# Optimization experiments

Measured on AMD Instinct MI355X. Metric: run time of the kernel, lower is better.

## Reference

```python
import jax, jax.numpy as jnp
import numpy as np

K = 3  # kernel_size

def setup_inputs() -> dict:
    key = jax.random.key(0)
    k1, k2, k3 = jax.random.split(key, 3)
    B, C, H, W = 8, 64, 128, 128
    x = jax.random.normal(k1, (B, C, H, W), dtype=jnp.float32)
    # 1x1 conv weight (out_channels*K*K, in_channels) and bias
    W_gen = jax.random.normal(k2, (C * K * K, C), dtype=jnp.float32) / np.float32(np.sqrt(C))
    b_gen = jax.random.normal(k3, (C * K * K,), dtype=jnp.float32) * 0.01
    return {"x": x, "W_gen": W_gen, "b_gen": b_gen}

def reference(x, W_gen, b_gen):
    B, C, H, W = x.shape  # out_channels == in_channels (required by the view)
    # filter_gen: 1x1 conv + ReLU -> (B, C*K*K, H, W)
    f = jax.nn.relu(jnp.einsum('bchw,oc->bohw', x, W_gen) + b_gen[None, :, None, None])
    filters = f.reshape(B, C, K * K, H, W)
    # F.unfold with padding=(K-1)//2, stride 1: gather KxK patches per pixel.
    pad = (K - 1) // 2
    xp = jnp.pad(x, ((0, 0), (0, 0), (pad, pad), (pad, pad)))
    # kernel-position index runs row-major (i*K + j), matching unfold layout
    patches = jnp.stack([xp[:, :, i:i + H, j:j + W]
                         for i in range(K) for j in range(K)], axis=2)  # (B,C,K*K,H,W)
    out = (filters * patches).sum(axis=2)  # (B,C,H,W)
    return out
```

## Files before the change

kernel.cpp:

```cpp
#include <hip/hip_runtime.h>
#include <hip/hip_bf16.h>

#define CC 64
#define HH 128
#define WW 128
#define OO 576
#define HW (HH * WW)

typedef __attribute__((ext_vector_type(8))) short short8;
typedef __attribute__((ext_vector_type(4))) short short4v;
typedef __attribute__((ext_vector_type(4))) float floatx4;

__device__ __forceinline__ unsigned short f2bf(float f) {
    unsigned u = __float_as_uint(f);
    u = (u + 0x7FFFu + ((u >> 16) & 1u)) >> 16;
    return (unsigned short)u;
}

__device__ __forceinline__ float bf2f(short s) {
    return __uint_as_float(((unsigned)(unsigned short)s) << 16);
}

__device__ __forceinline__ short8 pack8(floatx4 a, floatx4 b) {
    __hip_bfloat162 p0 = __float22bfloat162_rn(make_float2(a[0], a[1]));
    __hip_bfloat162 p1 = __float22bfloat162_rn(make_float2(a[2], a[3]));
    __hip_bfloat162 p2 = __float22bfloat162_rn(make_float2(b[0], b[1]));
    __hip_bfloat162 p3 = __float22bfloat162_rn(make_float2(b[2], b[3]));
    unsigned u0, u1, u2, u3;
    __builtin_memcpy(&u0, &p0, 4); __builtin_memcpy(&u1, &p1, 4);
    __builtin_memcpy(&u2, &p2, 4); __builtin_memcpy(&u3, &p3, 4);
    short8 v;
    v[0] = (short)(u0 & 0xffffu); v[1] = (short)(u0 >> 16);
    v[2] = (short)(u1 & 0xffffu); v[3] = (short)(u1 >> 16);
    v[4] = (short)(u2 & 0xffffu); v[5] = (short)(u2 >> 16);
    v[6] = (short)(u3 & 0xffffu); v[7] = (short)(u3 >> 16);
    return v;
}

__global__ void ACDA_wconv_kernel(const float* __restrict__ Wg,
                                  const float* __restrict__ bg,
                                  unsigned short* __restrict__ Wb,
                                  float* __restrict__ Bp) {
    int i = blockIdx.x * 256 + threadIdx.x;
    if (i < OO * CC) {
        int o2  = i >> 6;
        int col = i & 63;
        int kk  = o2 >> 6;
        int c   = o2 & 63;
        Wb[i] = f2bf(Wg[(c * 9 + kk) * CC + col]);
    }
    if (i < OO) Bp[i] = bg[(i & 63) * 9 + (i >> 6)];
}

__global__ __launch_bounds__(512, 4) void ACDA_main_kernel(
    const float* __restrict__ x, const unsigned short* __restrict__ Wb,
    const float* __restrict__ Bp, float* __restrict__ out)
{
    __shared__ short S[4][66][72];

    const int tid  = threadIdx.x;
    const int lane = tid & 63;
    const int g    = tid >> 6;
    const int hw   = g & 1;
    const int cg   = g >> 1;
    const int quad = lane >> 4;
    const int l16  = lane & 15;
    const int c0   = cg * 16;

    const int bid = blockIdx.x;
    const int wk  = (bid & 7) * 128 + (bid >> 3);
    const int seg = wk & 1;
    const int hp  = (wk >> 1) & 63;
    const int b   = wk >> 7;
    const int w0  = seg << 6;
    const int h0  = hp << 1;

    const float* xb = x + (size_t)b * CC * HW;

#pragma unroll
    for (int r = 0; r < 4; ++r) {
        const int hh = h0 + r - 1;
        const bool oob = (hh < 0) || (hh > 127);
        const int hc = hh < 0 ? 0 : (hh > 127 ? 127 : hh);
        const float* src = xb + hc * WW + w0 + lane;
        const int c = g * 8;
        short8 v8 = short8{0, 0, 0, 0, 0, 0, 0, 0};
        if (!oob) {
            floatx4 va, vb;
            va[0] = src[(c + 0) * HW]; va[1] = src[(c + 1) * HW];
            va[2] = src[(c + 2) * HW]; va[3] = src[(c + 3) * HW];
            vb[0] = src[(c + 4) * HW]; vb[1] = src[(c + 5) * HW];
            vb[2] = src[(c + 6) * HW]; vb[3] = src[(c + 7) * HW];
            v8 = pack8(va, vb);
        }
        *(short8*)&S[r][lane + 1][c] = v8;
    }
    {
        const int r4   = tid >> 7;
        const int idx  = tid & 127;
        const int c    = idx >> 1;
        const int side = idx & 1;
        const int hh = h0 + r4 - 1;
        const bool oob = (hh < 0) || (hh > 127);
        const int hc = hh < 0 ? 0 : (hh > 127 ? 127 : hh);
        const int col = side ? (w0 + 64) : (w0 - 1);
        unsigned short v = 0;
        if (!oob && col >= 0 && col < WW)
            v = f2bf(xb[c * HW + hc * WW + col]);
        S[r4][side ? 65 : 0][c] = (short)v;
    }
    __syncthreads();

    short8 bfrag[4][2];
#pragma unroll
    for (int nt = 0; nt < 4; ++nt)
#pragma unroll
        for (int ks = 0; ks < 2; ++ks) {
            bfrag[nt][ks] = *(const short8*)&S[hw + 1][nt * 16 + l16 + 1][ks * 32 + quad * 8];
            asm volatile("" : "+v"(bfrag[nt][ks]));
        }

    floatx4 acc[4];
#pragma unroll
    for (int nt = 0; nt < 4; ++nt) acc[nt] = floatx4{0.f, 0.f, 0.f, 0.f};

#pragma unroll
    for (int t = 0; t < 9; ++t) {
        const int di = t / 3;
        const int dj = t - 3 * di;
        const unsigned short* wrow = Wb + (t * 64 + c0 + l16) * CC + quad * 8;
        short8 a0 = *(const short8*)(wrow);
        short8 a1 = *(const short8*)(wrow + 32);
        floatx4 bv = *(const floatx4*)(Bp + t * 64 + c0 + 4 * quad);
#pragma unroll
        for (int nt = 0; nt < 4; ++nt) {
            short4v ph = *(const short4v*)&S[hw + di][nt * 16 + l16 + dj][c0 + 4 * quad];
            floatx4 z = bv;
            z = __builtin_amdgcn_mfma_f32_16x16x32_bf16(a0, bfrag[nt][0], z, 0, 0, 0);
            z = __builtin_amdgcn_mfma_f32_16x16x32_bf16(a1, bfrag[nt][1], z, 0, 0, 0);
#pragma unroll
            for (int rg = 0; rg < 4; ++rg)
                acc[nt][rg] = fmaf(fmaxf(z[rg], 0.f), bf2f(ph[rg]), acc[nt][rg]);
        }
    }

    float* ob = out + (size_t)b * CC * HW + (h0 + hw) * WW + w0;
#pragma unroll
    for (int nt = 0; nt < 4; ++nt)
#pragma unroll
        for (int rg = 0; rg < 4; ++rg)
            ob[(c0 + 4 * quad + rg) * HW + nt * 16 + l16] = acc[nt][rg];
}

extern "C" void kernel_launch(void* const* d_in, const int* in_sizes, int n_in,
                              void* d_out, int out_size, void* d_ws, size_t ws_size,
                              hipStream_t stream) {
    const float* x  = (const float*)d_in[0];
    const float* Wg = (const float*)d_in[1];
    const float* bg = (const float*)d_in[2];
    float* out = (float*)d_out;
    unsigned short* Wb = (unsigned short*)d_ws;
    float* Bp = (float*)((char*)d_ws + OO * CC * 2);

    ACDA_wconv_kernel<<<dim3((OO * CC + 255) / 256), dim3(256), 0, stream>>>(Wg, bg, Wb, Bp);
    ACDA_main_kernel<<<dim3(8 * 64 * 2), dim3(512), 0, stream>>>(x, Wb, Bp, out);
}
```

Before: 108.2 us.

## Pre-transpose input to channels-last bf16 in a fused prep kernel

A preprocessing kernel now converts x from NCHW fp32 to NHWC bf16 in workspace, using a shared-memory transpose. The same launch also handles the weight and bias reordering. The main kernel then stages its halo tile with contiguous 16-byte loads instead of strided per-channel fp32 gathers and per-element halo loads. This costs an extra full read and write of x (in bf16) through global memory, which the main kernel's cheaper, more coalesced loads must outweigh.

```diff
diff --git a/kernel.cpp b/kernel.cpp
--- a/kernel.cpp
+++ b/kernel.cpp
@@ -10,6 +10,7 @@
 typedef __attribute__((ext_vector_type(8))) short short8;
 typedef __attribute__((ext_vector_type(4))) short short4v;
 typedef __attribute__((ext_vector_type(4))) float floatx4;
+typedef __attribute__((ext_vector_type(4))) unsigned int uint4v;
 
 __device__ __forceinline__ unsigned short f2bf(float f) {
     unsigned u = __float_as_uint(f);
@@ -21,39 +22,56 @@
     return __uint_as_float(((unsigned)(unsigned short)s) << 16);
 }
 
-__device__ __forceinline__ short8 pack8(floatx4 a, floatx4 b) {
-    __hip_bfloat162 p0 = __float22bfloat162_rn(make_float2(a[0], a[1]));
-    __hip_bfloat162 p1 = __float22bfloat162_rn(make_float2(a[2], a[3]));
-    __hip_bfloat162 p2 = __float22bfloat162_rn(make_float2(b[0], b[1]));
-    __hip_bfloat162 p3 = __float22bfloat162_rn(make_float2(b[2], b[3]));
-    unsigned u0, u1, u2, u3;
-    __builtin_memcpy(&u0, &p0, 4); __builtin_memcpy(&u1, &p1, 4);
-    __builtin_memcpy(&u2, &p2, 4); __builtin_memcpy(&u3, &p3, 4);
-    short8 v;
-    v[0] = (short)(u0 & 0xffffu); v[1] = (short)(u0 >> 16);
-    v[2] = (short)(u1 & 0xffffu); v[3] = (short)(u1 >> 16);
-    v[4] = (short)(u2 & 0xffffu); v[5] = (short)(u2 >> 16);
-    v[6] = (short)(u3 & 0xffffu); v[7] = (short)(u3 >> 16);
-    return v;
-}
+__global__ __launch_bounds__(256) void ACDA_pre_kernel(
+    const float* __restrict__ x, const float* __restrict__ Wg,
+    const float* __restrict__ bg, unsigned short* __restrict__ Wb,
+    float* __restrict__ Bp, unsigned short* __restrict__ xbf)
+{
+    const int bid = blockIdx.x, tid = threadIdx.x;
+    if (bid >= 1024) {
+        int i = (bid - 1024) * 256 + tid;
+        if (i < OO * CC) {
+            int o2  = i >> 6;
+            int col = i & 63;
+            int kk  = o2 >> 6;
+            int c   = o2 & 63;
+            Wb[i] = f2bf(Wg[(c * 9 + kk) * CC + col]);
+        }
+        if (i < OO) Bp[i] = bg[(i & 63) * 9 + (i >> 6)];
+        return;
+    }
+    const int b = bid >> 7, h = bid & 127;
+    __shared__ float T[64][132];
 
-__global__ void ACDA_wconv_kernel(const float* __restrict__ Wg,
-                                  const float* __restrict__ bg,
-                                  unsigned short* __restrict__ Wb,
-                                  float* __restrict__ Bp) {
-    int i = blockIdx.x * 256 + threadIdx.x;
-    if (i < OO * CC) {
-        int o2  = i >> 6;
-        int col = i & 63;
-        int kk  = o2 >> 6;
-        int c   = o2 & 63;
-        Wb[i] = f2bf(Wg[(c * 9 + kk) * CC + col]);
+    {
+        const int c = tid >> 2, q = tid & 3;
+        const float* sp = x + ((size_t)(b * CC + c) * HH + h) * WW + q * 32;
+#pragma unroll
+        for (int j = 0; j < 8; ++j)
+            *(floatx4*)&T[c][q * 32 + 4 * j] = *(const floatx4*)(sp + 4 * j);
     }
-    if (i < OO) Bp[i] = bg[(i & 63) * 9 + (i >> 6)];
+    __syncthreads();
+    {
+        const int w = tid >> 1, half = tid & 1;
+        unsigned u[16];
+#pragma unroll
+        for (int k = 0; k < 16; ++k) {
+            float f0 = T[half * 32 + 2 * k][w];
+            float f1 = T[half * 32 + 2 * k + 1][w];
+            __hip_bfloat162 p = __float22bfloat162_rn(make_float2(f0, f1));
+            __builtin_memcpy(&u[k], &p, 4);
+        }
+        unsigned short* dp = xbf + ((size_t)(b * HH + h) * WW + w) * CC + half * 32;
+#pragma unroll
+        for (int m = 0; m < 4; ++m) {
+            uint4v v = {u[4 * m], u[4 * m + 1], u[4 * m + 2], u[4 * m + 3]};
+            *(uint4v*)(dp + m * 8) = v;
+        }
+    }
 }
 
 __global__ __launch_bounds__(512, 4) void ACDA_main_kernel(
-    const float* __restrict__ x, const unsigned short* __restrict__ Wb,
+    const unsigned short* __restrict__ xbf, const unsigned short* __restrict__ Wb,
     const float* __restrict__ Bp, float* __restrict__ out)
 {
     __shared__ short S[4][66][72];
@@ -75,40 +93,25 @@
     const int w0  = seg << 6;
     const int h0  = hp << 1;
 
-    const float* xb = x + (size_t)b * CC * HW;
+    const unsigned short* xq = xbf + (size_t)b * (HH * WW * CC);
+
+#define STAGE_CHUNK(C16) do {                                               \
+        const int slot_ = (C16) >> 3, ch8_ = (C16) & 7;                     \
+        const int r_ = slot_ / 66;                                          \
+        const int s_ = slot_ - 66 * r_;                                     \
+        const int hh_ = h0 + r_ - 1;                                        \
+        const int w_  = w0 + s_ - 1;                                        \
+        short8 v_ = {0, 0, 0, 0, 0, 0, 0, 0};                               \
+        if ((unsigned)hh_ < 128u && (unsigned)w_ < 128u)                    \
+            v_ = *(const short8*)(xq + ((size_t)hh_ * WW + w_) * CC + ch8_ * 8); \
+        *(short8*)((char*)&S[0][0][0] + slot_ * 144 + ch8_ * 16) = v_;      \
+    } while (0)
 
 #pragma unroll
-    for (int r = 0; r < 4; ++r) {
-        const int hh = h0 + r - 1;
-        const bool oob = (hh < 0) || (hh > 127);
-        const int hc = hh < 0 ? 0 : (hh > 127 ? 127 : hh);
-        const float* src = xb + hc * WW + w0 + lane;
-        const int c = g * 8;
-        short8 v8 = short8{0, 0, 0, 0, 0, 0, 0, 0};
-        if (!oob) {
-            floatx4 va, vb;
-            va[0] = src[(c + 0) * HW]; va[1] = src[(c + 1) * HW];
-            va[2] = src[(c + 2) * HW]; va[3] = src[(c + 3) * HW];
-            vb[0] = src[(c + 4) * HW]; vb[1] = src[(c + 5) * HW];
-            vb[2] = src[(c + 6) * HW]; vb[3] = src[(c + 7) * HW];
-            v8 = pack8(va, vb);
-        }
-        *(short8*)&S[r][lane + 1][c] = v8;
-    }
-    {
-        const int r4   = tid >> 7;
-        const int idx  = tid & 127;
-        const int c    = idx >> 1;
-        const int side = idx & 1;
-        const int hh = h0 + r4 - 1;
-        const bool oob = (hh < 0) || (hh > 127);
-        const int hc = hh < 0 ? 0 : (hh > 127 ? 127 : hh);
-        const int col = side ? (w0 + 64) : (w0 - 1);
-        unsigned short v = 0;
-        if (!oob && col >= 0 && col < WW)
-            v = f2bf(xb[c * HW + hc * WW + col]);
-        S[r4][side ? 65 : 0][c] = (short)v;
-    }
+    for (int j = 0; j < 4; ++j) STAGE_CHUNK(tid + j * 512);
+    if (tid < 64) STAGE_CHUNK(2048 + tid);
+#undef STAGE_CHUNK
+
     __syncthreads();
 
     short8 bfrag[4][2];
@@ -159,9 +162,10 @@
     const float* Wg = (const float*)d_in[1];
     const float* bg = (const float*)d_in[2];
     float* out = (float*)d_out;
-    unsigned short* Wb = (unsigned short*)d_ws;
-    float* Bp = (float*)((char*)d_ws + OO * CC * 2);
+    unsigned short* Wb  = (unsigned short*)d_ws;
+    float* Bp           = (float*)((char*)d_ws + OO * CC * 2);
+    unsigned short* xbf = (unsigned short*)((char*)d_ws + 131072);
 
-    ACDA_wconv_kernel<<<dim3((OO * CC + 255) / 256), dim3(256), 0, stream>>>(Wg, bg, Wb, Bp);
-    ACDA_main_kernel<<<dim3(8 * 64 * 2), dim3(512), 0, stream>>>(x, Wb, Bp, out);
+    ACDA_pre_kernel<<<dim3(1024 + 144), dim3(256), 0, stream>>>(x, Wg, bg, Wb, Bp, xbf);
+    ACDA_main_kernel<<<dim3(8 * 64 * 2), dim3(512), 0, stream>>>(xbf, Wb, Bp, out);
 }
```

Measured after the change: 114.2 us. 5.5% more time.
